# Kernel optimization log

Hardware: AMD Instinct MI355X
Metric: run time of the kernel (lower is better)

Reference implementation:

```python
import math
import jax
import jax.numpy as jnp
import numpy as np

SEGMENT_SIZE = 2048   # w (init: segment_size)
DILATION_RATE = 4     # r (init: dilation_rate)
D_MODEL = 1024        # init: d_model


def _sparse_indices(n: int, w: int, r: int, head_idx: int) -> np.ndarray:
    """Static SparsifyIndices: per segment of size w, take tokens offset::r.
    Since r divides w, every segment yields exactly m=w//r indices (no -1 pad).
    Returns flat global token indices, shape (S*m,)."""
    S = n // w
    m = w // r
    off = head_idx % r
    seg_start = np.arange(S, dtype=np.int64)[:, None] * w      # (S,1)
    within = off + r * np.arange(m, dtype=np.int64)[None, :]   # (1,m)
    return (seg_start + within).reshape(-1)


def setup_inputs() -> dict:
    key = jax.random.key(0)
    x = jax.random.normal(key, (4, 8192, D_MODEL), dtype=jnp.float32)
    return {"x": x, "head_idx": 1}


def reference(x, head_idx):
    b, n0, d = x.shape
    w, r = SEGMENT_SIZE, DILATION_RATE
    pad = (-n0) % w
    if pad:
        x = jnp.pad(x, ((0, 0), (0, pad), (0, 0)))
    n = n0 + pad
    idx = _sparse_indices(n, w, r, int(head_idx))  # static, (S*m,)
    S, m = n // w, w // r

    # Gather dilated tokens per segment: (b, S, m, d)
    xg = x[:, idx, :].reshape(b, S, m, d)

    # Softmax attention within each sub-segment (q=k=v=xg)
    scores = jnp.einsum('bsid,bsjd->bsij', xg, xg) / math.sqrt(d)  # (b,S,m,m)
    probs = jax.nn.softmax(scores, axis=-1)
    att = jnp.einsum('bsij,bsjd->bsid', probs, xg).reshape(b, S * m, d)

    # MixOutputs: alpha-weighted scatter-add back to full sequence
    denoms = att.sum(-1)                                       # (b, S*m)
    denom_sums = jnp.zeros((b, n), x.dtype).at[:, idx].add(denoms)
    alphas = denoms / denom_sums[:, idx]                       # (b, S*m)
    out = jnp.zeros((b, n, d), x.dtype).at[:, idx, :].add(att * alphas[..., None])
    return out
```

## Files before the change

kernel.cpp:

```cpp
#include <hip/hip_runtime.h>
#include <hip/hip_bf16.h>


typedef __bf16 bf16_t;
typedef __bf16 bf16x8 __attribute__((ext_vector_type(8)));
typedef float floatx4 __attribute__((ext_vector_type(4)));

#define D_MODEL 1024
#define SEG_W   2048
#define RATE    4
#define M_SUB   512
#define NTOK    8192
#define NSEGT   16
#define XG_ELEMS ((long)NSEGT * M_SUB * D_MODEL)

__device__ __forceinline__ void gload16(const bf16_t* g, bf16_t* l) {
    __builtin_amdgcn_global_load_lds(
        (const __attribute__((address_space(1))) void*)g,
        (__attribute__((address_space(3))) void*)l, 16, 0, 0);
}

__global__ __launch_bounds__(256) void gather_kernel(
    const float* __restrict__ x, const int* __restrict__ hidp,
    bf16_t* __restrict__ xg, bf16_t* __restrict__ xgT)
{
    const int off = ((hidp[0] % RATE) + RATE) % RATE;
    const int bid = blockIdx.x;
    const int seg = bid >> 7;
    const int rem = bid & 127;
    const int it  = rem >> 4;
    const int dt  = rem & 15;
    const int b   = seg >> 2, s = seg & 3;

    __shared__ ushort tile[64][65];

    const int t  = threadIdx.x;
    const int r  = t >> 2;
    const int cq = (t & 3) << 4;

    union U8 { bf16x8 v; ushort u[8]; };

    {
        const int  i   = it * 64 + r;
        const long tok = (long)s * SEG_W + off + 4L * i;
        const float* src = x + ((long)b * NTOK + tok) * D_MODEL + dt * 64 + cq;
        float4 f0 = ((const float4*)src)[0];
        float4 f1 = ((const float4*)src)[1];
        float4 f2 = ((const float4*)src)[2];
        float4 f3 = ((const float4*)src)[3];
        U8 lo, hi;
        lo.v[0]=(bf16_t)f0.x; lo.v[1]=(bf16_t)f0.y; lo.v[2]=(bf16_t)f0.z; lo.v[3]=(bf16_t)f0.w;
        lo.v[4]=(bf16_t)f1.x; lo.v[5]=(bf16_t)f1.y; lo.v[6]=(bf16_t)f1.z; lo.v[7]=(bf16_t)f1.w;
        hi.v[0]=(bf16_t)f2.x; hi.v[1]=(bf16_t)f2.y; hi.v[2]=(bf16_t)f2.z; hi.v[3]=(bf16_t)f2.w;
        hi.v[4]=(bf16_t)f3.x; hi.v[5]=(bf16_t)f3.y; hi.v[6]=(bf16_t)f3.z; hi.v[7]=(bf16_t)f3.w;
        bf16_t* dstg = xg + ((long)seg * M_SUB + i) * D_MODEL + dt * 64 + cq;
        *(bf16x8*)(dstg)     = lo.v;
        *(bf16x8*)(dstg + 8) = hi.v;
        #pragma unroll
        for (int j = 0; j < 8; ++j) { tile[r][cq + j] = lo.u[j]; tile[r][cq + 8 + j] = hi.u[j]; }
    }
    __syncthreads();
    {
        const int dc = r;
        const int iq = cq;
        U8 o0, o1;
        #pragma unroll
        for (int j = 0; j < 8; ++j) { o0.u[j] = tile[iq + j][dc]; o1.u[j] = tile[iq + 8 + j][dc]; }
        bf16_t* dstT = xgT + ((long)seg * D_MODEL + dt * 64 + dc) * M_SUB + it * 64 + iq;
        *(bf16x8*)(dstT)     = o0.v;
        *(bf16x8*)(dstT + 8) = o1.v;
    }
}

__global__ __launch_bounds__(256) void qk_kernel(
    const bf16_t* __restrict__ xg, bf16_t* __restrict__ S)
{
    const int bid = blockIdx.x;
    const int seg = bid >> 5;
    const int mt  = (bid >> 2) & 7;
    const int nt  = bid & 3;

    const int tid  = threadIdx.x;
    const int w    = tid >> 6;
    const int lane = tid & 63;
    const int l16  = lane & 15;
    const int quad = lane >> 4;
    const int wr   = w >> 1, wc = w & 1;
    const int rowin = lane >> 3;
    const int cswz  = ((lane & 7) ^ rowin) * 8;
    const int rsw   = l16 & 7;

    __shared__ alignas(16) bf16_t As[64 * 64];
    __shared__ alignas(16) bf16_t Bs[128 * 64];

    const bf16_t* xseg = xg + (long)seg * M_SUB * D_MODEL;

    const bf16_t* ga0 = xseg + (long)(mt * 64 + w * 16 + rowin) * D_MODEL + cswz;
    const bf16_t* ga1 = ga0 + 8 * D_MODEL;
    const bf16_t* gb0 = xseg + (long)(nt * 128 + w * 32 + rowin) * D_MODEL + cswz;
    const bf16_t* gb1 = gb0 +  8 * D_MODEL;
    const bf16_t* gb2 = gb0 + 16 * D_MODEL;
    const bf16_t* gb3 = gb0 + 24 * D_MODEL;
    bf16_t* la0 = &As[(w * 16 + 0) * 64];
    bf16_t* la1 = &As[(w * 16 + 8) * 64];
    bf16_t* lb0 = &Bs[(w * 32 + 0) * 64];
    bf16_t* lb1 = &Bs[(w * 32 + 8) * 64];
    bf16_t* lb2 = &Bs[(w * 32 + 16) * 64];
    bf16_t* lb3 = &Bs[(w * 32 + 24) * 64];

    floatx4 acc[2][4];
    #pragma unroll
    for (int i = 0; i < 2; ++i)
        #pragma unroll
        for (int j = 0; j < 4; ++j) acc[i][j] = (floatx4){0.f, 0.f, 0.f, 0.f};

    for (int kk = 0; kk < D_MODEL; kk += 64) {
        __syncthreads();
        gload16(ga0 + kk, la0); gload16(ga1 + kk, la1);
        gload16(gb0 + kk, lb0); gload16(gb1 + kk, lb1);
        gload16(gb2 + kk, lb2); gload16(gb3 + kk, lb3);
        __syncthreads();

        #pragma unroll
        for (int ks = 0; ks < 2; ++ks) {
            bf16x8 Af[2], Bf[4];
            #pragma unroll
            for (int m2 = 0; m2 < 2; ++m2) {
                const int row = wr * 32 + m2 * 16 + l16;
                Af[m2] = *(const bf16x8*)&As[row * 64 + (((ks * 4 + quad) ^ rsw) * 8)];
            }
            #pragma unroll
            for (int n2 = 0; n2 < 4; ++n2) {
                const int row = wc * 64 + n2 * 16 + l16;
                Bf[n2] = *(const bf16x8*)&Bs[row * 64 + (((ks * 4 + quad) ^ rsw) * 8)];
            }
            #pragma unroll
            for (int m2 = 0; m2 < 2; ++m2)
                #pragma unroll
                for (int n2 = 0; n2 < 4; ++n2)
                    acc[m2][n2] = __builtin_amdgcn_mfma_f32_16x16x32_bf16(Af[m2], Bf[n2], acc[m2][n2], 0, 0, 0);
        }
    }

    const float scale = 0.03125f;
    bf16_t* Sseg = S + (long)seg * M_SUB * M_SUB;
    #pragma unroll
    for (int m2 = 0; m2 < 2; ++m2) {
        const int qrow = mt * 64 + wr * 32 + m2 * 16 + quad * 4;
        #pragma unroll
        for (int n2 = 0; n2 < 4; ++n2) {
            const int col = nt * 128 + wc * 64 + n2 * 16 + l16;
            #pragma unroll
            for (int rg = 0; rg < 4; ++rg)
                Sseg[(long)(qrow + rg) * M_SUB + col] = (bf16_t)(acc[m2][n2][rg] * scale);
        }
    }
}

__global__ __launch_bounds__(256) void softmax_kernel(bf16_t* __restrict__ S)
{
    const int row  = blockIdx.x * 4 + (threadIdx.x >> 6);
    const int lane = threadIdx.x & 63;
    bf16_t* p = S + (long)row * M_SUB + lane * 8;
    bf16x8 v = *(const bf16x8*)p;
    float f[8];
    #pragma unroll
    for (int j = 0; j < 8; ++j) f[j] = (float)v[j];
    float m = f[0];
    #pragma unroll
    for (int j = 1; j < 8; ++j) m = fmaxf(m, f[j]);
    #pragma unroll
    for (int d = 1; d < 64; d <<= 1) m = fmaxf(m, __shfl_xor(m, d, 64));
    float sum = 0.f;
    #pragma unroll
    for (int j = 0; j < 8; ++j) { f[j] = __expf(f[j] - m); sum += f[j]; }
    #pragma unroll
    for (int d = 1; d < 64; d <<= 1) sum += __shfl_xor(sum, d, 64);
    const float inv = 1.0f / sum;
    #pragma unroll
    for (int j = 0; j < 8; ++j) v[j] = (bf16_t)(f[j] * inv);
    *(bf16x8*)p = v;
}

__global__ __launch_bounds__(256) void pv_kernel(
    const bf16_t* __restrict__ S, const bf16_t* __restrict__ xgT,
    const int* __restrict__ hidp, float* __restrict__ out)
{
    const int off = ((hidp[0] % RATE) + RATE) % RATE;
    const int bid = blockIdx.x;
    const int seg = bid >> 5;
    const int mt  = (bid >> 3) & 3;
    const int nt  = bid & 7;
    const int b   = seg >> 2, s = seg & 3;

    const int tid  = threadIdx.x;
    const int w    = tid >> 6;
    const int lane = tid & 63;
    const int l16  = lane & 15;
    const int quad = lane >> 4;
    const int wr   = w >> 1, wc = w & 1;
    const int rowin = lane >> 3;
    const int cswz  = ((lane & 7) ^ rowin) * 8;
    const int rsw   = l16 & 7;

    __shared__ alignas(16) bf16_t As[128 * 64];
    __shared__ alignas(16) bf16_t Bs[128 * 64];

    const bf16_t* Aseg = S   + (long)seg * M_SUB * M_SUB  + (long)mt * 128 * M_SUB;
    const bf16_t* Bseg = xgT + (long)seg * D_MODEL * M_SUB + (long)nt * 128 * M_SUB;

    const bf16_t* ga0 = Aseg + (long)(w * 32 + rowin) * M_SUB + cswz;
    const bf16_t* ga1 = ga0 +  8 * M_SUB;
    const bf16_t* ga2 = ga0 + 16 * M_SUB;
    const bf16_t* ga3 = ga0 + 24 * M_SUB;
    const bf16_t* gb0 = Bseg + (long)(w * 32 + rowin) * M_SUB + cswz;
    const bf16_t* gb1 = gb0 +  8 * M_SUB;
    const bf16_t* gb2 = gb0 + 16 * M_SUB;
    const bf16_t* gb3 = gb0 + 24 * M_SUB;
    bf16_t* la0 = &As[(w * 32 + 0) * 64];
    bf16_t* la1 = &As[(w * 32 + 8) * 64];
    bf16_t* la2 = &As[(w * 32 + 16) * 64];
    bf16_t* la3 = &As[(w * 32 + 24) * 64];
    bf16_t* lb0 = &Bs[(w * 32 + 0) * 64];
    bf16_t* lb1 = &Bs[(w * 32 + 8) * 64];
    bf16_t* lb2 = &Bs[(w * 32 + 16) * 64];
    bf16_t* lb3 = &Bs[(w * 32 + 24) * 64];

    floatx4 acc[4][4];
    #pragma unroll
    for (int i = 0; i < 4; ++i)
        #pragma unroll
        for (int j = 0; j < 4; ++j) acc[i][j] = (floatx4){0.f, 0.f, 0.f, 0.f};

    for (int kk = 0; kk < M_SUB; kk += 64) {
        __syncthreads();
        gload16(ga0 + kk, la0); gload16(ga1 + kk, la1);
        gload16(ga2 + kk, la2); gload16(ga3 + kk, la3);
        gload16(gb0 + kk, lb0); gload16(gb1 + kk, lb1);
        gload16(gb2 + kk, lb2); gload16(gb3 + kk, lb3);
        __syncthreads();

        #pragma unroll
        for (int ks = 0; ks < 2; ++ks) {
            bf16x8 Af[4], Bf[4];
            #pragma unroll
            for (int m2 = 0; m2 < 4; ++m2) {
                const int row = wr * 64 + m2 * 16 + l16;
                Af[m2] = *(const bf16x8*)&As[row * 64 + (((ks * 4 + quad) ^ rsw) * 8)];
            }
            #pragma unroll
            for (int n2 = 0; n2 < 4; ++n2) {
                const int row = wc * 64 + n2 * 16 + l16;
                Bf[n2] = *(const bf16x8*)&Bs[row * 64 + (((ks * 4 + quad) ^ rsw) * 8)];
            }
            #pragma unroll
            for (int m2 = 0; m2 < 4; ++m2)
                #pragma unroll
                for (int n2 = 0; n2 < 4; ++n2)
                    acc[m2][n2] = __builtin_amdgcn_mfma_f32_16x16x32_bf16(Af[m2], Bf[n2], acc[m2][n2], 0, 0, 0);
        }
    }

    float* obase = out + (long)b * NTOK * D_MODEL;
    #pragma unroll
    for (int m2 = 0; m2 < 4; ++m2) {
        const int qrow0 = mt * 128 + wr * 64 + m2 * 16 + quad * 4;
        #pragma unroll
        for (int rg = 0; rg < 4; ++rg) {
            const long tok = (long)s * SEG_W + off + 4L * (qrow0 + rg);
            float* orow = obase + tok * D_MODEL;
            #pragma unroll
            for (int n2 = 0; n2 < 4; ++n2) {
                const int d = nt * 128 + wc * 64 + n2 * 16 + l16;
                __builtin_nontemporal_store(acc[m2][n2][rg], &orow[d]);
            }
        }
    }

    {
        const floatx4 z = {0.f, 0.f, 0.f, 0.f};
        const int zr = tid >> 5;
        const int zc = tid & 31;
        #pragma unroll 4
        for (int p = 0; p < 48; ++p) {
            const int j = p * 8 + zr;
            const int q = j / 3, e = j % 3;
            const int delta = e + (e >= off ? 1 : 0);
            const long tok = (long)s * SEG_W + 4L * (mt * 128 + q) + delta;
            float* dst = obase + tok * D_MODEL + nt * 128 + zc * 4;
            __builtin_nontemporal_store(z, (floatx4*)dst);
        }
    }
}

extern "C" void kernel_launch(void* const* d_in, const int* in_sizes, int n_in,
                              void* d_out, int out_size, void* d_ws, size_t ws_size,
                              hipStream_t stream) {
    const float* x   = (const float*)d_in[0];
    const int*   hid = (const int*)d_in[1];
    float*       out = (float*)d_out;
    bf16_t* xg  = (bf16_t*)d_ws;
    bf16_t* xgT = xg + XG_ELEMS;
    bf16_t* S   = xgT + XG_ELEMS;

    gather_kernel<<<dim3(2048), dim3(256), 0, stream>>>(x, hid, xg, xgT);
    qk_kernel<<<dim3(512), dim3(256), 0, stream>>>(xg, S);
    softmax_kernel<<<dim3(2048), dim3(256), 0, stream>>>(S);
    pv_kernel<<<dim3(512), dim3(256), 0, stream>>>(S, xgT, hid, out);
}
```

Measured before the change: 248.5 us.

## Fuse softmax into PV kernel with full score row-tile held in LDS

Removes the separate softmax kernel. Each PV block now loads a 64x512 tile of raw scores into LDS, normalises the rows in place, and then runs the PV matmul against that resident tile. M-tiles shrink from 128 to 64 rows and the grid doubles to 1024 blocks. This saves a kernel launch and one read-write round trip of the score matrix. In exchange, softmax is recomputed once per column tile (8 times per row), and the larger LDS footprint (about 80KB) may lower occupancy.

New measurement: 250.8 us. No clear change (+0.9%).

```diff
diff --git a/kernel.cpp b/kernel.cpp
--- a/kernel.cpp
+++ b/kernel.cpp
@@ -157,39 +157,14 @@
     }
 }
 
-__global__ __launch_bounds__(256) void softmax_kernel(bf16_t* __restrict__ S)
-{
-    const int row  = blockIdx.x * 4 + (threadIdx.x >> 6);
-    const int lane = threadIdx.x & 63;
-    bf16_t* p = S + (long)row * M_SUB + lane * 8;
-    bf16x8 v = *(const bf16x8*)p;
-    float f[8];
-    #pragma unroll
-    for (int j = 0; j < 8; ++j) f[j] = (float)v[j];
-    float m = f[0];
-    #pragma unroll
-    for (int j = 1; j < 8; ++j) m = fmaxf(m, f[j]);
-    #pragma unroll
-    for (int d = 1; d < 64; d <<= 1) m = fmaxf(m, __shfl_xor(m, d, 64));
-    float sum = 0.f;
-    #pragma unroll
-    for (int j = 0; j < 8; ++j) { f[j] = __expf(f[j] - m); sum += f[j]; }
-    #pragma unroll
-    for (int d = 1; d < 64; d <<= 1) sum += __shfl_xor(sum, d, 64);
-    const float inv = 1.0f / sum;
-    #pragma unroll
-    for (int j = 0; j < 8; ++j) v[j] = (bf16_t)(f[j] * inv);
-    *(bf16x8*)p = v;
-}
-
-__global__ __launch_bounds__(256) void pv_kernel(
+__global__ __launch_bounds__(256) void pv_fused_kernel(
     const bf16_t* __restrict__ S, const bf16_t* __restrict__ xgT,
     const int* __restrict__ hidp, float* __restrict__ out)
 {
     const int off = ((hidp[0] % RATE) + RATE) % RATE;
     const int bid = blockIdx.x;
-    const int seg = bid >> 5;
-    const int mt  = (bid >> 3) & 3;
+    const int seg = bid >> 6;
+    const int mt  = (bid >> 3) & 7;
     const int nt  = bid & 7;
     const int b   = seg >> 2, s = seg & 3;
 
@@ -203,50 +178,80 @@
     const int cswz  = ((lane & 7) ^ rowin) * 8;
     const int rsw   = l16 & 7;
 
-    __shared__ alignas(16) bf16_t As[128 * 64];
+    __shared__ alignas(16) bf16_t Stile[64 * 512];
     __shared__ alignas(16) bf16_t Bs[128 * 64];
 
-    const bf16_t* Aseg = S   + (long)seg * M_SUB * M_SUB  + (long)mt * 128 * M_SUB;
+    const bf16_t* Srow0 = S + (long)seg * M_SUB * M_SUB + (long)(mt * 64) * M_SUB;
+    #pragma unroll
+    for (int i = 0; i < 16; ++i) {
+        const int row = w * 16 + i;
+        const bf16_t* g = Srow0 + (long)row * M_SUB + ((lane ^ (i & 7)) * 8);
+        gload16(g, &Stile[row * 512]);
+    }
+    __syncthreads();
+
+    {
+        const int sub = lane >> 5;
+        const int c   = lane & 31;
+        #pragma unroll
+        for (int pass = 0; pass < 8; ++pass) {
+            const int row = w * 16 + pass * 2 + sub;
+            bf16_t* p0 = &Stile[row * 512 + c * 8];
+            bf16_t* p1 = &Stile[row * 512 + (c + 32) * 8];
+            bf16x8 v0 = *(const bf16x8*)p0;
+            bf16x8 v1 = *(const bf16x8*)p1;
+            float f[16];
+            #pragma unroll
+            for (int j = 0; j < 8; ++j) { f[j] = (float)v0[j]; f[8 + j] = (float)v1[j]; }
+            float m = f[0];
+            #pragma unroll
+            for (int j = 1; j < 16; ++j) m = fmaxf(m, f[j]);
+            #pragma unroll
+            for (int d = 1; d < 32; d <<= 1) m = fmaxf(m, __shfl_xor(m, d, 64));
+            float sum = 0.f;
+            #pragma unroll
+            for (int j = 0; j < 16; ++j) { f[j] = __expf(f[j] - m); sum += f[j]; }
+            #pragma unroll
+            for (int d = 1; d < 32; d <<= 1) sum += __shfl_xor(sum, d, 64);
+            const float inv = 1.0f / sum;
+            #pragma unroll
+            for (int j = 0; j < 8; ++j) { v0[j] = (bf16_t)(f[j] * inv); v1[j] = (bf16_t)(f[8 + j] * inv); }
+            *(bf16x8*)p0 = v0;
+            *(bf16x8*)p1 = v1;
+        }
+    }
+    __syncthreads();
+
     const bf16_t* Bseg = xgT + (long)seg * D_MODEL * M_SUB + (long)nt * 128 * M_SUB;
-
-    const bf16_t* ga0 = Aseg + (long)(w * 32 + rowin) * M_SUB + cswz;
-    const bf16_t* ga1 = ga0 +  8 * M_SUB;
-    const bf16_t* ga2 = ga0 + 16 * M_SUB;
-    const bf16_t* ga3 = ga0 + 24 * M_SUB;
     const bf16_t* gb0 = Bseg + (long)(w * 32 + rowin) * M_SUB + cswz;
     const bf16_t* gb1 = gb0 +  8 * M_SUB;
     const bf16_t* gb2 = gb0 + 16 * M_SUB;
     const bf16_t* gb3 = gb0 + 24 * M_SUB;
-    bf16_t* la0 = &As[(w * 32 + 0) * 64];
-    bf16_t* la1 = &As[(w * 32 + 8) * 64];
-    bf16_t* la2 = &As[(w * 32 + 16) * 64];
-    bf16_t* la3 = &As[(w * 32 + 24) * 64];
     bf16_t* lb0 = &Bs[(w * 32 + 0) * 64];
     bf16_t* lb1 = &Bs[(w * 32 + 8) * 64];
     bf16_t* lb2 = &Bs[(w * 32 + 16) * 64];
     bf16_t* lb3 = &Bs[(w * 32 + 24) * 64];
 
-    floatx4 acc[4][4];
-    #pragma unroll
-    for (int i = 0; i < 4; ++i)
+    floatx4 acc[2][4];
+    #pragma unroll
+    for (int i = 0; i < 2; ++i)
         #pragma unroll
         for (int j = 0; j < 4; ++j) acc[i][j] = (floatx4){0.f, 0.f, 0.f, 0.f};
 
     for (int kk = 0; kk < M_SUB; kk += 64) {
         __syncthreads();
-        gload16(ga0 + kk, la0); gload16(ga1 + kk, la1);
-        gload16(ga2 + kk, la2); gload16(ga3 + kk, la3);
         gload16(gb0 + kk, lb0); gload16(gb1 + kk, lb1);
         gload16(gb2 + kk, lb2); gload16(gb3 + kk, lb3);
         __syncthreads();
 
+        const int kchunk = kk >> 3;
         #pragma unroll
         for (int ks = 0; ks < 2; ++ks) {
-            bf16x8 Af[4], Bf[4];
-            #pragma unroll
-            for (int m2 = 0; m2 < 4; ++m2) {
-                const int row = wr * 64 + m2 * 16 + l16;
-                Af[m2] = *(const bf16x8*)&As[row * 64 + (((ks * 4 + quad) ^ rsw) * 8)];
+            bf16x8 Af[2], Bf[4];
+            #pragma unroll
+            for (int m2 = 0; m2 < 2; ++m2) {
+                const int row = wr * 32 + m2 * 16 + l16;
+                Af[m2] = *(const bf16x8*)&Stile[row * 512 + (kchunk | ((ks * 4 + quad) ^ rsw)) * 8];
             }
             #pragma unroll
             for (int n2 = 0; n2 < 4; ++n2) {
@@ -254,7 +259,7 @@
                 Bf[n2] = *(const bf16x8*)&Bs[row * 64 + (((ks * 4 + quad) ^ rsw) * 8)];
             }
             #pragma unroll
-            for (int m2 = 0; m2 < 4; ++m2)
+            for (int m2 = 0; m2 < 2; ++m2)
                 #pragma unroll
                 for (int n2 = 0; n2 < 4; ++n2)
                     acc[m2][n2] = __builtin_amdgcn_mfma_f32_16x16x32_bf16(Af[m2], Bf[n2], acc[m2][n2], 0, 0, 0);
@@ -263,8 +268,8 @@
 
     float* obase = out + (long)b * NTOK * D_MODEL;
     #pragma unroll
-    for (int m2 = 0; m2 < 4; ++m2) {
-        const int qrow0 = mt * 128 + wr * 64 + m2 * 16 + quad * 4;
+    for (int m2 = 0; m2 < 2; ++m2) {
+        const int qrow0 = mt * 64 + wr * 32 + m2 * 16 + quad * 4;
         #pragma unroll
         for (int rg = 0; rg < 4; ++rg) {
             const long tok = (long)s * SEG_W + off + 4L * (qrow0 + rg);
@@ -282,11 +287,11 @@
         const int zr = tid >> 5;
         const int zc = tid & 31;
         #pragma unroll 4
-        for (int p = 0; p < 48; ++p) {
+        for (int p = 0; p < 24; ++p) {
             const int j = p * 8 + zr;
             const int q = j / 3, e = j % 3;
             const int delta = e + (e >= off ? 1 : 0);
-            const long tok = (long)s * SEG_W + 4L * (mt * 128 + q) + delta;
+            const long tok = (long)s * SEG_W + 4L * (mt * 64 + q) + delta;
             float* dst = obase + tok * D_MODEL + nt * 128 + zc * 4;
             __builtin_nontemporal_store(z, (floatx4*)dst);
         }
@@ -305,6 +310,5 @@
 
     gather_kernel<<<dim3(2048), dim3(256), 0, stream>>>(x, hid, xg, xgT);
     qk_kernel<<<dim3(512), dim3(256), 0, stream>>>(xg, S);
-    softmax_kernel<<<dim3(2048), dim3(256), 0, stream>>>(S);
-    pv_kernel<<<dim3(512), dim3(256), 0, stream>>>(S, xgT, hid, out);
-}
+    pv_fused_kernel<<<dim3(1024), dim3(256), 0, stream>>>(S, xgT, hid, out);
+}
```
